# Optimization experiments

Hardware: AMD Instinct MI355X
Metric: run time of the kernel (lower is better)

Reference implementation:

```python
import jax, jax.numpy as jnp
import numpy as np

D_EMB = 1024
N_HEADS = 16


def setup_inputs() -> dict:
    key = jax.random.key(0)
    k_x, k_wq, k_bq, k_wp, k_bp = jax.random.split(key, 5)
    B, N, D = 8, 1024, D_EMB
    x = jax.random.normal(k_x, (B, N, D), dtype=jnp.float32)
    s = 1.0 / np.sqrt(D)
    w_qkv = jax.random.normal(k_wq, (D, 3 * D), dtype=jnp.float32) * s
    b_qkv = jax.random.normal(k_bq, (3 * D,), dtype=jnp.float32) * 0.01
    w_proj = jax.random.normal(k_wp, (D, D), dtype=jnp.float32) * s
    b_proj = jax.random.normal(k_bp, (D,), dtype=jnp.float32) * 0.01
    return {"x": x, "w_qkv": w_qkv, "b_qkv": b_qkv, "w_proj": w_proj, "b_proj": b_proj}


def reference(x, w_qkv, b_qkv, w_proj, b_proj):
    B, N, D = x.shape
    H = N_HEADS
    d = D // H
    qkv = x @ w_qkv + b_qkv                      # [B, N, 3D]
    # einops '(h d qkv)': qkv index is the innermost factor of the last dim
    qkv = qkv.reshape(B, N, H, d, 3)
    q = qkv[..., 0]                              # [B, N, H, d]
    k = qkv[..., 1]
    v = qkv[..., 2]
    score = jnp.einsum('bqhd,bkhd->bhqk', q, k)  # [B, H, N, N]
    # module scales AFTER softmax, by sqrt(d_emb) (not sqrt(d_head))
    att = jax.nn.softmax(score, axis=-1) / jnp.sqrt(jnp.float32(D))
    out = jnp.einsum('bhqk,bkhd->bqhd', att, v).reshape(B, N, D)
    return out @ w_proj + b_proj
```

## Files before the change

kernel.cpp:

```cpp
#include <hip/hip_runtime.h>
#include <hip/hip_bf16.h>
#include <stdint.h>

typedef __hip_bfloat16 bf16;
typedef __attribute__((ext_vector_type(8))) short short8;
typedef __attribute__((ext_vector_type(4))) float f32x4;
typedef __attribute__((ext_vector_type(16))) float f32x16;

#define MFMA16(a, b, c) __builtin_amdgcn_mfma_f32_16x16x32_bf16(a, b, c, 0, 0, 0)
#define MFMA32(a, b, c) __builtin_amdgcn_mfma_f32_32x32x16_bf16(a, b, c, 0, 0, 0)

#define BATCH 8
#define SEQ   1024
#define DEMB  1024
#define NH    16
#define DH    64
#define MTOT  (BATCH * SEQ)
#define LOG2E 1.44269504088896340736f

__device__ __forceinline__ float rdf(const void* p, size_t idx, int isf) {
  if (isf) return ((const float*)p)[idx];
  return __bfloat162float(((const bf16*)p)[idx]);
}

__device__ __forceinline__ unsigned int pk2(float a, float b) {
  unsigned short ua = __bfloat16_as_ushort(__float2bfloat16(a));
  unsigned short ub = __bfloat16_as_ushort(__float2bfloat16(b));
  return (unsigned int)ua | ((unsigned int)ub << 16);
}

union U4S8 { uint4 u; short8 s; };

__device__ __forceinline__ void gload16(const bf16* g, bf16* l) {
  __builtin_amdgcn_global_load_lds(
      (const __attribute__((address_space(1))) void*)g,
      (__attribute__((address_space(3))) void*)l, 16, 0, 0);
}

__global__ void detect_dtype(const unsigned int* __restrict__ xw, int* __restrict__ flag) {
  int lane = threadIdx.x;
  float v = __uint_as_float(xw[lane]);
  bool isf32 = (fabsf(v) < 1e20f);
  unsigned long long m = __ballot(isf32);
  if (lane == 0) flag[0] = (__popcll(m) >= 32) ? 1 : 0;
}

__global__ __launch_bounds__(256) void convert_x(
    const void* __restrict__ xin, bf16* __restrict__ xc, const int* __restrict__ flag) {
  const int isf = flag[0];
  size_t i = ((size_t)blockIdx.x * 256 + threadIdx.x) * 8;
  if (isf) {
    const float* xf = (const float*)xin;
    float4 a = *(const float4*)&xf[i];
    float4 b = *(const float4*)&xf[i + 4];
    bf16 o[8];
    o[0] = __float2bfloat16(a.x); o[1] = __float2bfloat16(a.y);
    o[2] = __float2bfloat16(a.z); o[3] = __float2bfloat16(a.w);
    o[4] = __float2bfloat16(b.x); o[5] = __float2bfloat16(b.y);
    o[6] = __float2bfloat16(b.z); o[7] = __float2bfloat16(b.w);
    *(int4*)&xc[i] = *(const int4*)&o[0];
  } else {
    *(int4*)&xc[i] = *(const int4*)&((const bf16*)xin)[i];
  }
}

__global__ __launch_bounds__(256) void permute_wqkv(
    const void* __restrict__ w, const void* __restrict__ b,
    bf16* __restrict__ wt, float* __restrict__ bqp, const int* __restrict__ flag) {
  __shared__ __attribute__((aligned(16))) bf16 ls[192][66];
  const int isf = flag[0];
  const int t = threadIdx.x;
  const int k0 = blockIdx.x * 64;
  const int h = blockIdx.y;
#pragma unroll
  for (int i = 0; i < 48; ++i) {
    int e = t + i * 256;
    int k = e / 192, c = e % 192;
    ls[c][k] = __float2bfloat16(rdf(w, (size_t)(k0 + k) * 3072 + h * 192 + c, isf));
  }
  if (blockIdx.x == 0 && t < 192) {
    int dd = t / 3, j = t % 3;
    bqp[j * 1024 + h * 64 + dd] = rdf(b, h * 192 + t, isf);
  }
  __syncthreads();
#pragma unroll
  for (int i = 0; i < 48; ++i) {
    int e = t + i * 256;
    int c = e / 64, k = e & 63;
    int dd = c / 3, j = c % 3;
    wt[(size_t)(j * 1024 + h * 64 + dd) * 1024 + k0 + k] = ls[c][k];
  }
}

__global__ __launch_bounds__(256) void transpose_wp(
    const void* __restrict__ w, bf16* __restrict__ wt, const int* __restrict__ flag) {
  __shared__ __attribute__((aligned(16))) bf16 ls[64][66];
  const int isf = flag[0];
  const int t = threadIdx.x;
  const int r0 = blockIdx.y * 64;
  const int c0 = blockIdx.x * 64;
#pragma unroll
  for (int i = 0; i < 16; ++i) {
    int e = t + i * 256;
    int r = e >> 6, c = e & 63;
    ls[c][r] = __float2bfloat16(rdf(w, (size_t)(r0 + r) * 1024 + c0 + c, isf));
  }
  __syncthreads();
#pragma unroll
  for (int i = 0; i < 16; ++i) {
    int e = t + i * 256;
    int c = e >> 6, r = e & 63;
    wt[(size_t)(c0 + c) * 1024 + r0 + r] = ls[c][r];
  }
}

#define RSLOT 12288
__device__ __forceinline__ void gemm128x256_core(
    const bf16* __restrict__ A, const bf16* __restrict__ Bt,
    int m0, int n0, bf16* lds, f32x4 acc[4][4]) {
  const int t = threadIdx.x;
  const int lane = t & 63, w = t >> 6;
  const int l15 = lane & 15, quad = lane >> 4;
  const int wm = w >> 2, wn = w & 3;
  const int sr = lane >> 2;
  const int scs = (((lane & 3) ^ ((lane >> 3) & 3))) * 8;
  const bf16* gA = A + (size_t)(m0 + w * 16 + sr) * 1024 + scs;
  const bf16* gB = Bt + (size_t)(n0 + w * 16 + sr) * 1024 + scs;

#pragma unroll
  for (int tt = 0; tt < 4; ++tt) {
    bf16* sb = lds + tt * RSLOT;
    gload16(gA + tt * 32, sb + w * 512);
    gload16(gB + tt * 32, sb + 4096 + w * 512);
    gload16(gB + tt * 32 + 131072, sb + 4096 + 4096 + w * 512);
  }
  asm volatile("s_waitcnt vmcnt(9)" ::: "memory");
  __builtin_amdgcn_s_barrier();
  asm volatile("" ::: "memory");

  const int swz8 = ((quad ^ (l15 >> 1)) & 3) * 8;
  const int paOff = (wm * 64 + l15) * 32 + swz8;
  const int pbOff = 4096 + (wn * 64 + l15) * 32 + swz8;

  int sl = 0;
  int sp = 4;
  int kp = 128;

  for (int tau = 0; tau < 32; ++tau) {
    const bf16* pa = lds + sl * RSLOT + paOff;
    const bf16* pb = lds + sl * RSLOT + pbOff;
    short8 afr[4], bfr[4];
#pragma unroll
    for (int i = 0; i < 4; ++i) afr[i] = *(const short8*)(pa + i * 512);
#pragma unroll
    for (int j = 0; j < 4; ++j) bfr[j] = *(const short8*)(pb + j * 512);
    bf16* sb = lds + sp * RSLOT;
    gload16(gA + kp, sb + w * 512);
    gload16(gB + kp, sb + 4096 + w * 512);
    gload16(gB + kp + 131072, sb + 4096 + 4096 + w * 512);
    asm volatile("" ::: "memory");
    __builtin_amdgcn_s_barrier();
    asm volatile("s_waitcnt lgkmcnt(0)" ::: "memory");
    __builtin_amdgcn_s_setprio(1);
#pragma unroll
    for (int i = 0; i < 4; ++i)
#pragma unroll
      for (int j = 0; j < 4; ++j)
        acc[i][j] = MFMA16(afr[i], bfr[j], acc[i][j]);
    __builtin_amdgcn_s_setprio(0);
    asm volatile("s_waitcnt vmcnt(9)" ::: "memory");
    __builtin_amdgcn_s_barrier();
    asm volatile("" ::: "memory");
    sl = (sl == 4) ? 0 : sl + 1;
    sp = (sp == 4) ? 0 : sp + 1;
    kp = (kp + 32) & 1023;
  }
  asm volatile("s_waitcnt vmcnt(0)" ::: "memory");
}

__global__ __launch_bounds__(512, 2) void gemm_qkv(
    const bf16* __restrict__ A, const bf16* __restrict__ Bt,
    const float* __restrict__ bias,
    bf16* __restrict__ qb, bf16* __restrict__ kb, bf16* __restrict__ vb) {
  extern __shared__ bf16 smem[];
  const int t = threadIdx.x;
  const int lane = t & 63;
  const int l15 = lane & 15, quad = lane >> 4;
  const int w = t >> 6, wm = w >> 2, wn = w & 3;
  const int bid = blockIdx.x;
  const int swz = (bid & 7) * 96 + (bid >> 3);
  const int m0 = (swz / 12) * 128;
  const int n0 = (swz % 12) * 256;

  f32x4 acc[4][4];
  const f32x4 zero = {0.f, 0.f, 0.f, 0.f};
#pragma unroll
  for (int i = 0; i < 4; ++i)
#pragma unroll
    for (int j = 0; j < 4; ++j) acc[i][j] = zero;

  gemm128x256_core(A, Bt, m0, n0, smem, acc);

  const int jj = n0 >> 10;
  const int hh = ((n0 + wn * 64) & 1023) >> 6;
  const float qscale = (jj == 0) ? LOG2E : 1.0f;
#pragma unroll
  for (int fi = 0; fi < 4; ++fi) {
    int m = m0 + wm * 64 + fi * 16 + quad * 4;
    int bb = m >> 10, nidx = m & 1023;
    size_t bhq = (size_t)(bb * NH + hh);
#pragma unroll
    for (int fj = 0; fj < 4; ++fj) {
      int dd = fj * 16 + l15;
      float bv = bias[n0 + wn * 64 + dd];
      if (jj == 2) {
        unsigned int lo = pk2(acc[fi][fj][0] + bv, acc[fi][fj][1] + bv);
        unsigned int hi = pk2(acc[fi][fj][2] + bv, acc[fi][fj][3] + bv);
        *(uint2*)&vb[(bhq * 64 + dd) * 1024 + nidx] = make_uint2(lo, hi);
      } else {
        bf16* dst = (jj == 0) ? qb : kb;
#pragma unroll
        for (int r = 0; r < 4; ++r)
          dst[(bhq * 1024 + (size_t)(nidx + r)) * 64 + dd] =
              __float2bfloat16((acc[fi][fj][r] + bv) * qscale);
      }
    }
  }
}

__global__ __launch_bounds__(256, 4) void attn(
    const bf16* __restrict__ qb, const bf16* __restrict__ kb,
    const bf16* __restrict__ vb, bf16* __restrict__ ob) {
  const int t = threadIdx.x, lane = t & 63, w = t >> 6;
  const int q5 = lane & 31, half = lane >> 5;
  const int bh = blockIdx.y;
  const int bat = bh >> 4, h = bh & 15;
  const int q0 = blockIdx.x * 128;
  const int qrow = q0 + w * 32 + q5;

  __shared__ __attribute__((aligned(16))) bf16 lsK[64][72];
  __shared__ __attribute__((aligned(16))) bf16 lsV[64][72];

  const bf16* qp = qb + (size_t)bh * (1024 * 64);
  const bf16* kp = kb + (size_t)bh * (1024 * 64);
  const bf16* vp = vb + (size_t)bh * (64 * 1024);

  short8 bq[4];
#pragma unroll
  for (int kk = 0; kk < 4; ++kk)
    bq[kk] = *(const short8*)&qp[(size_t)qrow * 64 + kk * 16 + half * 8];

  float l_run = 0.f;
  f32x16 po[2];
#pragma unroll
  for (int r = 0; r < 16; ++r) { po[0][r] = 0.f; po[1][r] = 0.f; }

  const int sr = t >> 3;
  const int sc = (t & 7) * 8;

  int4 g0 = *(const int4*)&kp[(size_t)sr * 64 + sc];
  int4 g1 = *(const int4*)&kp[(size_t)(32 + sr) * 64 + sc];
  int4 g2 = *(const int4*)&vp[(size_t)sr * 1024 + sc];
  int4 g3 = *(const int4*)&vp[(size_t)(32 + sr) * 1024 + sc];

  for (int kt = 0; kt < 1024; kt += 64) {
    __syncthreads();
    *(int4*)&lsK[sr][sc] = g0;
    *(int4*)&lsK[32 + sr][sc] = g1;
    *(int4*)&lsV[sr][sc] = g2;
    *(int4*)&lsV[32 + sr][sc] = g3;
    __syncthreads();

    const int ktn = kt + 64;
    if (ktn < 1024) {
      g0 = *(const int4*)&kp[(size_t)(ktn + sr) * 64 + sc];
      g1 = *(const int4*)&kp[(size_t)(ktn + 32 + sr) * 64 + sc];
      g2 = *(const int4*)&vp[(size_t)sr * 1024 + ktn + sc];
      g3 = *(const int4*)&vp[(size_t)(32 + sr) * 1024 + ktn + sc];
    }

    f32x16 st[2];
#pragma unroll
    for (int r = 0; r < 16; ++r) { st[0][r] = 0.f; st[1][r] = 0.f; }
#pragma unroll
    for (int kk = 0; kk < 4; ++kk) {
#pragma unroll
      for (int tj = 0; tj < 2; ++tj) {
        short8 ak = *(const short8*)&lsK[tj * 32 + q5][kk * 16 + half * 8];
        st[tj] = MFMA32(ak, bq[kk], st[tj]);
      }
    }

    float lsum = 0.f;
#pragma unroll
    for (int tj = 0; tj < 2; ++tj)
#pragma unroll
      for (int r = 0; r < 16; ++r) {
        float p = exp2f(st[tj][r]);
        st[tj][r] = p;
        lsum += p;
      }
    l_run += lsum;

#pragma unroll
    for (int kk2 = 0; kk2 < 4; ++kk2) {
      const int nbA = 2 * kk2, nbB = 2 * kk2 + 1;
      unsigned int a0 = pk2(st[nbA >> 2][4 * (nbA & 3) + 0], st[nbA >> 2][4 * (nbA & 3) + 1]);
      unsigned int a1 = pk2(st[nbA >> 2][4 * (nbA & 3) + 2], st[nbA >> 2][4 * (nbA & 3) + 3]);
      unsigned int b0 = pk2(st[nbB >> 2][4 * (nbB & 3) + 0], st[nbB >> 2][4 * (nbB & 3) + 1]);
      unsigned int b1 = pk2(st[nbB >> 2][4 * (nbB & 3) + 2], st[nbB >> 2][4 * (nbB & 3) + 3]);
      unsigned int s0 = half ? a0 : b0;
      unsigned int s1 = half ? a1 : b1;
      unsigned int r0 = (unsigned int)__shfl_xor((int)s0, 32);
      unsigned int r1 = (unsigned int)__shfl_xor((int)s1, 32);
      U4S8 fr;
      fr.u.x = half ? r0 : a0;
      fr.u.y = half ? r1 : a1;
      fr.u.z = half ? b0 : r0;
      fr.u.w = half ? b1 : r1;
#pragma unroll
      for (int ti = 0; ti < 2; ++ti) {
        short8 av = *(const short8*)&lsV[ti * 32 + q5][kk2 * 16 + half * 8];
        po[ti] = MFMA32(av, fr.s, po[ti]);
      }
    }
  }

  l_run += __shfl_xor(l_run, 32);
  float inv = 1.0f / (l_run * 32.0f);
  bf16* op = ob + ((size_t)(bat * 1024 + qrow)) * 1024 + h * 64;
#pragma unroll
  for (int ti = 0; ti < 2; ++ti)
#pragma unroll
    for (int g = 0; g < 4; ++g) {
      unsigned int lo = pk2(po[ti][4 * g + 0] * inv, po[ti][4 * g + 1] * inv);
      unsigned int hi = pk2(po[ti][4 * g + 2] * inv, po[ti][4 * g + 3] * inv);
      uint2 u = make_uint2(lo, hi);
      *(uint2*)&op[ti * 32 + g * 8 + half * 4] = u;
    }
}

__global__ __launch_bounds__(512, 2) void gemm_proj(
    const bf16* __restrict__ A, const bf16* __restrict__ Bt,
    const void* __restrict__ bias, float* __restrict__ out,
    const int* __restrict__ flag) {
  extern __shared__ bf16 smem[];
  const int t = threadIdx.x;
  const int lane = t & 63;
  const int l15 = lane & 15, quad = lane >> 4;
  const int w = t >> 6, wm = w >> 2, wn = w & 3;
  const int bid = blockIdx.x;
  const int swz = (bid & 7) * 32 + (bid >> 3);
  const int m0 = (swz >> 2) * 128;
  const int n0 = (swz & 3) * 256;

  f32x4 acc[4][4];
  const f32x4 zero = {0.f, 0.f, 0.f, 0.f};
#pragma unroll
  for (int i = 0; i < 4; ++i)
#pragma unroll
    for (int j = 0; j < 4; ++j) acc[i][j] = zero;

  gemm128x256_core(A, Bt, m0, n0, smem, acc);

  const int isf = flag[0];
#pragma unroll
  for (int fj = 0; fj < 4; ++fj) {
    int c = n0 + wn * 64 + fj * 16 + l15;
    float bv = rdf(bias, c, isf);
#pragma unroll
    for (int fi = 0; fi < 4; ++fi) {
      int m = m0 + wm * 64 + fi * 16 + quad * 4;
#pragma unroll
      for (int r = 0; r < 4; ++r)
        out[(size_t)(m + r) * 1024 + c] = acc[fi][fj][r] + bv;
    }
  }
}

extern "C" void kernel_launch(void* const* d_in, const int* in_sizes, int n_in,
                              void* d_out, int out_size, void* d_ws, size_t ws_size,
                              hipStream_t stream) {
  const void* x      = d_in[0];
  const void* w_qkv  = d_in[1];
  const void* b_qkv  = d_in[2];
  const void* w_proj = d_in[3];
  const void* b_proj = d_in[4];
  float* out = (float*)d_out;

  char* ws = (char*)d_ws;
  bf16*  wt_qkv = (bf16*)(ws);
  float* bqp    = (float*)(ws + 6291456);
  bf16*  wtp    = (bf16*)(ws + 6303744);
  bf16*  xc     = (bf16*)(ws + 8400896);
  bf16*  q_buf  = (bf16*)(ws + 25178112);
  bf16*  k_buf  = (bf16*)(ws + 41955328);
  bf16*  v_buf  = (bf16*)(ws + 58732544);
  int*   flag   = (int*)(ws + 75509760);
  bf16*  att    = xc;

  static bool lds_attr_done = false;
  if (!lds_attr_done) {
    (void)hipFuncSetAttribute(reinterpret_cast<const void*>(gemm_qkv),
                              hipFuncAttributeMaxDynamicSharedMemorySize, 122880);
    (void)hipFuncSetAttribute(reinterpret_cast<const void*>(gemm_proj),
                              hipFuncAttributeMaxDynamicSharedMemorySize, 122880);
    lds_attr_done = true;
  }

  detect_dtype<<<1, 64, 0, stream>>>((const unsigned int*)x, flag);
  convert_x<<<4096, 256, 0, stream>>>(x, xc, flag);
  permute_wqkv<<<dim3(16, 16), 256, 0, stream>>>(w_qkv, b_qkv, wt_qkv, bqp, flag);
  transpose_wp<<<dim3(16, 16), 256, 0, stream>>>(w_proj, wtp, flag);
  gemm_qkv<<<dim3(768), 512, 122880, stream>>>(xc, wt_qkv, bqp, q_buf, k_buf, v_buf);
  attn<<<dim3(8, 128), 256, 0, stream>>>(q_buf, k_buf, v_buf, att);
  gemm_proj<<<dim3(256), 512, 122880, stream>>>(att, wtp, b_proj, out, flag);
}
```

Measured before the change: 275.4 us.

## Enlarge QKV GEMM tile to 256x256 with split-phase prefetch pipeline

The QKV projection GEMM moves from 128x256 to 256x256 output tiles, so each block does twice the MFMA work per loaded B tile and the grid halves to 384 blocks. The K loop now uses a 4-slot LDS ring of 32 KB slots (128 KB total) and splits each step into two MFMA half-phases, issuing the A and B prefetches in separate phases to spread global traffic. The cost is 32 fp32 accumulators per lane instead of 16, which adds register pressure, and larger LDS use. With 131072 bytes per block only one block may fit per CU, so occupancy may drop below the launch bound of 2.

```diff
diff --git a/kernel.cpp b/kernel.cpp
--- a/kernel.cpp
+++ b/kernel.cpp
@@ -114,50 +114,50 @@
   }
 }
 
-#define RSLOT 12288
-__device__ __forceinline__ void gemm128x256_core(
+__device__ __forceinline__ void gemm256_core(
     const bf16* __restrict__ A, const bf16* __restrict__ Bt,
-    int m0, int n0, bf16* lds, f32x4 acc[4][4]) {
+    int m0, int n0, bf16* lds, f32x4 acc[8][4]) {
   const int t = threadIdx.x;
   const int lane = t & 63, w = t >> 6;
   const int l15 = lane & 15, quad = lane >> 4;
   const int wm = w >> 2, wn = w & 3;
+
   const int sr = lane >> 2;
   const int scs = (((lane & 3) ^ ((lane >> 3) & 3))) * 8;
   const bf16* gA = A + (size_t)(m0 + w * 16 + sr) * 1024 + scs;
   const bf16* gB = Bt + (size_t)(n0 + w * 16 + sr) * 1024 + scs;
 
 #pragma unroll
-  for (int tt = 0; tt < 4; ++tt) {
-    bf16* sb = lds + tt * RSLOT;
+  for (int tt = 0; tt < 3; ++tt) {
+    bf16* sb = lds + tt * 16384;
     gload16(gA + tt * 32, sb + w * 512);
-    gload16(gB + tt * 32, sb + 4096 + w * 512);
-    gload16(gB + tt * 32 + 131072, sb + 4096 + 4096 + w * 512);
-  }
-  asm volatile("s_waitcnt vmcnt(9)" ::: "memory");
+    gload16(gA + tt * 32 + 131072, sb + 4096 + w * 512);
+    gload16(gB + tt * 32, sb + 8192 + w * 512);
+    gload16(gB + tt * 32 + 131072, sb + 12288 + w * 512);
+  }
+  asm volatile("s_waitcnt vmcnt(8)" ::: "memory");
   __builtin_amdgcn_s_barrier();
-  asm volatile("" ::: "memory");
 
   const int swz8 = ((quad ^ (l15 >> 1)) & 3) * 8;
-  const int paOff = (wm * 64 + l15) * 32 + swz8;
-  const int pbOff = 4096 + (wn * 64 + l15) * 32 + swz8;
-
-  int sl = 0;
-  int sp = 4;
-  int kp = 128;
-
+  const bf16* paBase = lds + (wm * 128 + l15) * 32 + swz8;
+  const bf16* pbBase = lds + 8192 + (wn * 64 + l15) * 32 + swz8;
+
+#pragma unroll 4
   for (int tau = 0; tau < 32; ++tau) {
-    const bf16* pa = lds + sl * RSLOT + paOff;
-    const bf16* pb = lds + sl * RSLOT + pbOff;
+    const int slot = tau & 3;
+    const int pf = (tau + 3) & 3;
+    const int kpf = ((tau + 3) & 31) * 32;
+    const bf16* pa0 = paBase + slot * 16384;
+    const bf16* pb0 = pbBase + slot * 16384;
+    bf16* sb = lds + pf * 16384;
+
     short8 afr[4], bfr[4];
 #pragma unroll
-    for (int i = 0; i < 4; ++i) afr[i] = *(const short8*)(pa + i * 512);
-#pragma unroll
-    for (int j = 0; j < 4; ++j) bfr[j] = *(const short8*)(pb + j * 512);
-    bf16* sb = lds + sp * RSLOT;
-    gload16(gA + kp, sb + w * 512);
-    gload16(gB + kp, sb + 4096 + w * 512);
-    gload16(gB + kp + 131072, sb + 4096 + 4096 + w * 512);
+    for (int i = 0; i < 4; ++i) afr[i] = *(const short8*)(pa0 + i * 512);
+#pragma unroll
+    for (int j = 0; j < 4; ++j) bfr[j] = *(const short8*)(pb0 + j * 512);
+    gload16(gA + kpf, sb + w * 512);
+    gload16(gA + kpf + 131072, sb + 4096 + w * 512);
     asm volatile("" ::: "memory");
     __builtin_amdgcn_s_barrier();
     asm volatile("s_waitcnt lgkmcnt(0)" ::: "memory");
@@ -168,12 +168,27 @@
       for (int j = 0; j < 4; ++j)
         acc[i][j] = MFMA16(afr[i], bfr[j], acc[i][j]);
     __builtin_amdgcn_s_setprio(0);
-    asm volatile("s_waitcnt vmcnt(9)" ::: "memory");
-    __builtin_amdgcn_s_barrier();
-    asm volatile("" ::: "memory");
-    sl = (sl == 4) ? 0 : sl + 1;
-    sp = (sp == 4) ? 0 : sp + 1;
-    kp = (kp + 32) & 1023;
+    asm volatile("" ::: "memory");
+    __builtin_amdgcn_s_barrier();
+
+    const bf16* pa1 = pa0 + 64 * 32;
+#pragma unroll
+    for (int i = 0; i < 4; ++i) afr[i] = *(const short8*)(pa1 + i * 512);
+    gload16(gB + kpf, sb + 8192 + w * 512);
+    gload16(gB + kpf + 131072, sb + 12288 + w * 512);
+    asm volatile("" ::: "memory");
+    __builtin_amdgcn_s_barrier();
+    asm volatile("s_waitcnt lgkmcnt(0)" ::: "memory");
+    __builtin_amdgcn_s_setprio(1);
+#pragma unroll
+    for (int i = 0; i < 4; ++i)
+#pragma unroll
+      for (int j = 0; j < 4; ++j)
+        acc[4 + i][j] = MFMA16(afr[i], bfr[j], acc[4 + i][j]);
+    __builtin_amdgcn_s_setprio(0);
+    asm volatile("s_waitcnt vmcnt(8)" ::: "memory");
+    asm volatile("" ::: "memory");
+    __builtin_amdgcn_s_barrier();
   }
   asm volatile("s_waitcnt vmcnt(0)" ::: "memory");
 }
@@ -188,25 +203,25 @@
   const int l15 = lane & 15, quad = lane >> 4;
   const int w = t >> 6, wm = w >> 2, wn = w & 3;
   const int bid = blockIdx.x;
-  const int swz = (bid & 7) * 96 + (bid >> 3);
-  const int m0 = (swz / 12) * 128;
+  const int swz = (bid & 7) * 48 + (bid >> 3);
+  const int m0 = (swz / 12) * 256;
   const int n0 = (swz % 12) * 256;
 
-  f32x4 acc[4][4];
+  f32x4 acc[8][4];
   const f32x4 zero = {0.f, 0.f, 0.f, 0.f};
 #pragma unroll
-  for (int i = 0; i < 4; ++i)
+  for (int i = 0; i < 8; ++i)
 #pragma unroll
     for (int j = 0; j < 4; ++j) acc[i][j] = zero;
 
-  gemm128x256_core(A, Bt, m0, n0, smem, acc);
+  gemm256_core(A, Bt, m0, n0, smem, acc);
 
   const int jj = n0 >> 10;
   const int hh = ((n0 + wn * 64) & 1023) >> 6;
   const float qscale = (jj == 0) ? LOG2E : 1.0f;
 #pragma unroll
-  for (int fi = 0; fi < 4; ++fi) {
-    int m = m0 + wm * 64 + fi * 16 + quad * 4;
+  for (int fi = 0; fi < 8; ++fi) {
+    int m = m0 + wm * 128 + fi * 16 + quad * 4;
     int bb = m >> 10, nidx = m & 1023;
     size_t bhq = (size_t)(bb * NH + hh);
 #pragma unroll
@@ -340,6 +355,70 @@
     }
 }
 
+#define RSLOT 12288
+__device__ __forceinline__ void gemm128x256_core(
+    const bf16* __restrict__ A, const bf16* __restrict__ Bt,
+    int m0, int n0, bf16* lds, f32x4 acc[4][4]) {
+  const int t = threadIdx.x;
+  const int lane = t & 63, w = t >> 6;
+  const int l15 = lane & 15, quad = lane >> 4;
+  const int wm = w >> 2, wn = w & 3;
+  const int sr = lane >> 2;
+  const int scs = (((lane & 3) ^ ((lane >> 3) & 3))) * 8;
+  const bf16* gA = A + (size_t)(m0 + w * 16 + sr) * 1024 + scs;
+  const bf16* gB = Bt + (size_t)(n0 + w * 16 + sr) * 1024 + scs;
+
+#pragma unroll
+  for (int tt = 0; tt < 4; ++tt) {
+    bf16* sb = lds + tt * RSLOT;
+    gload16(gA + tt * 32, sb + w * 512);
+    gload16(gB + tt * 32, sb + 4096 + w * 512);
+    gload16(gB + tt * 32 + 131072, sb + 4096 + 4096 + w * 512);
+  }
+  asm volatile("s_waitcnt vmcnt(9)" ::: "memory");
+  __builtin_amdgcn_s_barrier();
+  asm volatile("" ::: "memory");
+
+  const int swz8 = ((quad ^ (l15 >> 1)) & 3) * 8;
+  const int paOff = (wm * 64 + l15) * 32 + swz8;
+  const int pbOff = 4096 + (wn * 64 + l15) * 32 + swz8;
+
+  int sl = 0;
+  int sp = 4;
+  int kp = 128;
+
+  for (int tau = 0; tau < 32; ++tau) {
+    const bf16* pa = lds + sl * RSLOT + paOff;
+    const bf16* pb = lds + sl * RSLOT + pbOff;
+    short8 afr[4], bfr[4];
+#pragma unroll
+    for (int i = 0; i < 4; ++i) afr[i] = *(const short8*)(pa + i * 512);
+#pragma unroll
+    for (int j = 0; j < 4; ++j) bfr[j] = *(const short8*)(pb + j * 512);
+    bf16* sb = lds + sp * RSLOT;
+    gload16(gA + kp, sb + w * 512);
+    gload16(gB + kp, sb + 4096 + w * 512);
+    gload16(gB + kp + 131072, sb + 4096 + 4096 + w * 512);
+    asm volatile("" ::: "memory");
+    __builtin_amdgcn_s_barrier();
+    asm volatile("s_waitcnt lgkmcnt(0)" ::: "memory");
+    __builtin_amdgcn_s_setprio(1);
+#pragma unroll
+    for (int i = 0; i < 4; ++i)
+#pragma unroll
+      for (int j = 0; j < 4; ++j)
+        acc[i][j] = MFMA16(afr[i], bfr[j], acc[i][j]);
+    __builtin_amdgcn_s_setprio(0);
+    asm volatile("s_waitcnt vmcnt(9)" ::: "memory");
+    __builtin_amdgcn_s_barrier();
+    asm volatile("" ::: "memory");
+    sl = (sl == 4) ? 0 : sl + 1;
+    sp = (sp == 4) ? 0 : sp + 1;
+    kp = (kp + 32) & 1023;
+  }
+  asm volatile("s_waitcnt vmcnt(0)" ::: "memory");
+}
+
 __global__ __launch_bounds__(512, 2) void gemm_proj(
     const bf16* __restrict__ A, const bf16* __restrict__ Bt,
     const void* __restrict__ bias, float* __restrict__ out,
@@ -402,7 +481,7 @@
   static bool lds_attr_done = false;
   if (!lds_attr_done) {
     (void)hipFuncSetAttribute(reinterpret_cast<const void*>(gemm_qkv),
-                              hipFuncAttributeMaxDynamicSharedMemorySize, 122880);
+                              hipFuncAttributeMaxDynamicSharedMemorySize, 131072);
     (void)hipFuncSetAttribute(reinterpret_cast<const void*>(gemm_proj),
                               hipFuncAttributeMaxDynamicSharedMemorySize, 122880);
     lds_attr_done = true;
@@ -412,7 +491,7 @@
   convert_x<<<4096, 256, 0, stream>>>(x, xc, flag);
   permute_wqkv<<<dim3(16, 16), 256, 0, stream>>>(w_qkv, b_qkv, wt_qkv, bqp, flag);
   transpose_wp<<<dim3(16, 16), 256, 0, stream>>>(w_proj, wtp, flag);
-  gemm_qkv<<<dim3(768), 512, 122880, stream>>>(xc, wt_qkv, bqp, q_buf, k_buf, v_buf);
+  gemm_qkv<<<dim3(384), 512, 131072, stream>>>(xc, wt_qkv, bqp, q_buf, k_buf, v_buf);
   attn<<<dim3(8, 128), 256, 0, stream>>>(q_buf, k_buf, v_buf, att);
   gemm_proj<<<dim3(256), 512, 122880, stream>>>(att, wtp, b_proj, out, flag);
 }
```

New measurement: 275.2 us. No clear change (-0.0%).
